# Kernel tuning notes

Measured on AMD Instinct MI355X. Metric: run time of the kernel, lower is better.

## Reference

```python
import jax, jax.numpy as jnp
import numpy as np

NH = 4
TEMP = 0.5

def _ln(x, w, b):
    mu = x.mean(-1, keepdims=True)
    var = ((x - mu) ** 2).mean(-1, keepdims=True)
    return (x - mu) / jnp.sqrt(var + 1e-5) * w + b

def _encoder(x, bias, key_pad, layers):
    # pre-LN torch TransformerEncoder, relu FFN, dropout=0
    Wqkv, bqkv, Wo, bo, ln1w, ln1b, ln2w, ln2b, W1, b1, W2, b2 = layers
    B, L, H = x.shape
    d = H // NH
    scale = 1.0 / np.sqrt(d)
    for i in range(Wqkv.shape[0]):
        y = _ln(x, ln1w[i], ln1b[i])
        qkv = y @ Wqkv[i].T + bqkv[i]
        q, k, v = jnp.split(qkv, 3, axis=-1)
        q = q.reshape(B, L, NH, d).transpose(0, 2, 1, 3)
        k = k.reshape(B, L, NH, d).transpose(0, 2, 1, 3)
        v = v.reshape(B, L, NH, d).transpose(0, 2, 1, 3)
        s = jnp.einsum('bhqd,bhkd->bhqk', q, k) * scale
        if bias is not None:
            s = s + bias
        s = s + key_pad[:, None, None, :]
        a = jax.nn.softmax(s, axis=-1)
        o = jnp.einsum('bhqk,bhkd->bhqd', a, v).transpose(0, 2, 1, 3).reshape(B, L, H)
        x = x + o @ Wo[i].T + bo[i]
        y = _ln(x, ln2w[i], ln2b[i])
        x = x + jax.nn.relu(y @ W1[i].T + b1[i]) @ W2[i].T + b2[i]
    return x

def _layer_params(key, nl, H, F, sc=0.05):
    ks = jax.random.split(key, 4)
    return (jax.random.normal(ks[0], (nl, 3 * H, H)) * sc, jnp.zeros((nl, 3 * H)),
            jax.random.normal(ks[1], (nl, H, H)) * sc, jnp.zeros((nl, H)),
            jnp.ones((nl, H)), jnp.zeros((nl, H)), jnp.ones((nl, H)), jnp.zeros((nl, H)),
            jax.random.normal(ks[2], (nl, F, H)) * sc, jnp.zeros((nl, F)),
            jax.random.normal(ks[3], (nl, H, F)) * sc, jnp.zeros((nl, H)))

def setup_inputs():
    key = jax.random.key(0)
    IN, H, ED, F = 64, 128, 16, 256
    G, NPG = 8, 512
    N = G * NPG
    m, k = 4, 16
    T = N
    S = T * m
    EPS = 24
    E_loc = S * EPS
    E = 65536
    ks = jax.random.split(key, 13)
    x = jax.random.normal(ks[0], (N, IN))
    log_probs = -jnp.abs(jax.random.normal(ks[1], (S,)))
    root = jnp.repeat(jnp.arange(T), m)
    base = (root // NPG) * NPG
    rest = base[:, None] + jax.random.randint(ks[2], (S, k - 1), 0, NPG)
    nodes_sampled = jnp.concatenate([root[:, None], rest], axis=1)
    valid = jnp.ones((S * k,), dtype=bool)
    edge_index_sampled = jax.random.randint(ks[3], (2, E_loc), 0, k)
    edge_ptr = jnp.arange(S + 1) * EPS
    ea_flat = jax.random.normal(ks[4], (E_loc, ED))
    src = jax.random.randint(ks[5], (E,), 0, N)
    dst = (src // NPG) * NPG + jax.random.randint(ks[6], (E,), 0, NPG)
    edge_index = jnp.stack([src, dst])
    edge_attr = jax.random.normal(ks[7], (E, ED))
    batch_vec = jnp.arange(N) // NPG
    ptr = jnp.arange(G + 1) * NPG
    d = dict(x=x, log_probs=log_probs, ea_flat=ea_flat, edge_attr=edge_attr,
             init_W=jax.random.normal(ks[8], (H, IN + 2)) * 0.05, init_b=jnp.zeros((H,)),
             loc_ep_W=jax.random.normal(ks[9], (NH, ED)) * 0.05, loc_ep_b=jnp.zeros((NH,)),
             glob_ep_W=jax.random.normal(ks[10], (NH, ED)) * 0.05, glob_ep_b=jnp.zeros((NH,)),
             loc_nw=jnp.ones((H,)), loc_nb=jnp.zeros((H,)),
             glob_nw=jnp.ones((H,)), glob_nb=jnp.zeros((H,)),
             nodes_sampled=nodes_sampled, edge_index_sampled=edge_index_sampled,
             edge_ptr=edge_ptr, edge_index=edge_index, batch_vec=batch_vec,
             ptr=ptr, valid=valid)
    names = ['Wqkv', 'bqkv', 'Wo', 'bo', 'ln1w', 'ln1b', 'ln2w', 'ln2b', 'W1', 'b1', 'W2', 'b2']
    for n, a in zip(names, _layer_params(ks[11], 4, H, F)):
        d['loc_' + n] = a
    for n, a in zip(names, _layer_params(ks[12], 4, H, F)):
        d['glob_' + n] = a
    return d

def reference(x, log_probs, ea_flat, edge_attr, init_W, init_b, loc_ep_W, loc_ep_b,
              glob_ep_W, glob_ep_b, loc_nw, loc_nb, glob_nw, glob_nb,
              loc_Wqkv, loc_bqkv, loc_Wo, loc_bo, loc_ln1w, loc_ln1b, loc_ln2w, loc_ln2b,
              loc_W1, loc_b1, loc_W2, loc_b2,
              glob_Wqkv, glob_bqkv, glob_Wo, glob_bo, glob_ln1w, glob_ln1b, glob_ln2w, glob_ln2b,
              glob_W1, glob_b1, glob_W2, glob_b2,
              nodes_sampled, edge_index_sampled, edge_ptr, edge_index, batch_vec, ptr, valid):
    S, k = nodes_sampled.shape
    N = x.shape[0]
    T = N
    m = S // T
    G = ptr.shape[0] - 1
    max_N = N // G  # equal-size graphs
    H = init_W.shape[0]
    # ---- phase 1: flatten subgraphs + init features ----
    x_flat = x[nodes_sampled.reshape(-1)]                         # [S*k, IN]
    root_global = jnp.repeat(jnp.arange(T), m)                    # [S]
    root_local = jnp.argmax(nodes_sampled == root_global[:, None], axis=1)
    root_mask = jnp.zeros((S * k,), x.dtype).at[jnp.arange(S) * k + root_local].set(1.0)
    lp = jnp.where(jnp.isfinite(log_probs), log_probs, 0.0)
    lp_flat = jnp.repeat(lp, k)[:, None] * valid[:, None].astype(x.dtype)
    h = jnp.concatenate([x_flat, lp_flat, root_mask[:, None]], axis=1) @ init_W.T + init_b
    # ---- local edge bias (scatter-add) ----
    E_loc = ea_flat.shape[0]
    sub = jnp.searchsorted(edge_ptr, jnp.arange(E_loc), side='right') - 1
    eap = ea_flat @ loc_ep_W.T + loc_ep_b                         # [E_loc, NH]
    lbias = jnp.zeros((S, k, k, NH), x.dtype).at[sub, edge_index_sampled[0], edge_index_sampled[1]].add(eap).transpose(0, 3, 1, 2)
    v2 = valid.reshape(S, k)
    key_pad_l = jnp.where(v2, 0.0, -1e9).astype(x.dtype)
    loc_layers = (loc_Wqkv, loc_bqkv, loc_Wo, loc_bo, loc_ln1w, loc_ln1b, loc_ln2w, loc_ln2b, loc_W1, loc_b1, loc_W2, loc_b2)
    out = _encoder(h.reshape(S, k, H), lbias, key_pad_l, loc_layers)
    out = _ln(out, loc_nw, loc_nb)
    vf = v2.astype(x.dtype)[..., None]
    sub_embs = (out * vf).sum(1) / jnp.maximum(vf.sum(1), 1.0)    # [S, H]
    # ---- weighted-mean aggregation over m samples per target node ----
    w = jax.nn.softmax(log_probs.reshape(T, m) / TEMP, axis=1)
    node_embs = jnp.einsum('tm,tmh->th', w, sub_embs.reshape(T, m, H))
    # ---- global phase: to_dense_batch + edge-bias transformer ----
    pos = jnp.arange(N) - ptr[batch_vec]
    dense = jnp.zeros((G, max_N, H), x.dtype).at[batch_vec, pos].set(node_embs)
    vmask = jnp.zeros((G, max_N), bool).at[batch_vec, pos].set(True)
    g = batch_vec[edge_index[0]]
    sl = edge_index[0] - ptr[g]
    dl = edge_index[1] - ptr[g]
    eag = edge_attr @ glob_ep_W.T + glob_ep_b
    gbias = jnp.zeros((G, max_N, max_N, NH), x.dtype).at[g, sl, dl].add(eag).transpose(0, 3, 1, 2)
    key_pad_g = jnp.where(vmask, 0.0, -1e9).astype(x.dtype)
    glob_layers = (glob_Wqkv, glob_bqkv, glob_Wo, glob_bo, glob_ln1w, glob_ln1b, glob_ln2w, glob_ln2b, glob_W1, glob_b1, glob_W2, glob_b2)
    gout = _encoder(dense, gbias, key_pad_g, glob_layers)
    gout = _ln(gout, glob_nw, glob_nb)
    return (gout * vmask[..., None].astype(x.dtype)).sum(1)      # [G, H]
```

## Files before the change

kernel.cpp:

```cpp
#include <hip/hip_runtime.h>
#include <math.h>

#define IN_F      64
#define H_DIM     128
#define NH_       4
#define DH_       32
#define FF_DIM    256
#define KSUB      16
#define S_SEQ     16384
#define E_LOC     393216
#define G_NUM     8
#define NPG_      512
#define N_NODES   4096
#define E_GLOB    65536
#define NLAYERS   4
#define SCALE_ATT 0.17677669529663687f

#define WQKV_SZ   (3*H_DIM*H_DIM)
#define WO_SZ     (H_DIM*H_DIM)
#define W1_SZ     (FF_DIM*H_DIM)
#define W2_SZ     (H_DIM*FF_DIM)

#define ATT(sg)   (4352 + (sg) * 2560)
#define PS_OFF    9472
#define STG_SZ    10112

typedef __bf16 bf16x8 __attribute__((ext_vector_type(8)));
typedef float  f32x4  __attribute__((ext_vector_type(4)));

__device__ __forceinline__ unsigned short f2bf(float f) {
    unsigned u = __float_as_uint(f);
    unsigned r = (u + 0x7fffu + ((u >> 16) & 1u)) >> 16;
    return (unsigned short)r;
}

__device__ __forceinline__ unsigned cvt_pk(float lo, float hi) {
    unsigned r;
    asm("v_cvt_pk_bf16_f32 %0, %1, %2" : "=v"(r) : "v"(lo), "v"(hi));
    return r;
}

__device__ __forceinline__ f32x4 mfma16(bf16x8 a, bf16x8 b, f32x4 c) {
    return __builtin_amdgcn_mfma_f32_16x16x32_bf16(a, b, c, 0, 0, 0);
}

#define PRIO_HI() __builtin_amdgcn_s_setprio(1)
#define PRIO_LO() __builtin_amdgcn_s_setprio(0)

__device__ __forceinline__ void ln_to_row(const float (&X)[8][4],
    const float* __restrict__ w, const float* __restrict__ b,
    unsigned short* rowb, int r, int q)
{
    float s1[4] = {0,0,0,0}, s2[4] = {0,0,0,0};
    #pragma unroll
    for (int t = 0; t < 8; ++t)
        #pragma unroll
        for (int i = 0; i < 4; ++i) { float v = X[t][i]; s1[i] += v; s2[i] += v*v; }
    #pragma unroll
    for (int i = 0; i < 4; ++i) {
        float a = s1[i], c = s2[i];
        a += __shfl_xor(a, 1, 16); a += __shfl_xor(a, 2, 16);
        a += __shfl_xor(a, 4, 16); a += __shfl_xor(a, 8, 16);
        c += __shfl_xor(c, 1, 16); c += __shfl_xor(c, 2, 16);
        c += __shfl_xor(c, 4, 16); c += __shfl_xor(c, 8, 16);
        float mu = a * (1.f / H_DIM);
        float var = c * (1.f / H_DIM) - mu * mu;
        s1[i] = mu; s2[i] = rsqrtf(fmaxf(var, 0.f) + 1e-5f);
    }
    for (int t = 0; t < 8; ++t) {
        float wv = w[t * 16 + r], bv = b[t * 16 + r];
        float v0 = (X[t][0] - s1[0]) * s2[0] * wv + bv;
        float v1 = (X[t][1] - s1[1]) * s2[1] * wv + bv;
        float v2 = (X[t][2] - s1[2]) * s2[2] * wv + bv;
        float v3 = (X[t][3] - s1[3]) * s2[3] * wv + bv;
        unsigned lo = cvt_pk(v0, v1), hi = cvt_pk(v2, v3);
        rowb[(q * 4 + 0) * 136 + t * 16 + r] = (unsigned short)lo;
        rowb[(q * 4 + 1) * 136 + t * 16 + r] = (unsigned short)(lo >> 16);
        rowb[(q * 4 + 2) * 136 + t * 16 + r] = (unsigned short)hi;
        rowb[(q * 4 + 3) * 136 + t * 16 + r] = (unsigned short)(hi >> 16);
    }
}

__device__ __forceinline__ void ln_mean_out(const float (&X)[8][4],
    const float* __restrict__ fnw, const float* __restrict__ fnb,
    float* __restrict__ dst, int r, int q)
{
    float s1[4] = {0,0,0,0}, s2[4] = {0,0,0,0};
    #pragma unroll
    for (int t = 0; t < 8; ++t)
        #pragma unroll
        for (int i = 0; i < 4; ++i) { float v = X[t][i]; s1[i] += v; s2[i] += v*v; }
    #pragma unroll
    for (int i = 0; i < 4; ++i) {
        float a = s1[i], c = s2[i];
        a += __shfl_xor(a, 1, 16); a += __shfl_xor(a, 2, 16);
        a += __shfl_xor(a, 4, 16); a += __shfl_xor(a, 8, 16);
        c += __shfl_xor(c, 1, 16); c += __shfl_xor(c, 2, 16);
        c += __shfl_xor(c, 4, 16); c += __shfl_xor(c, 8, 16);
        float mu = a * (1.f / H_DIM);
        float var = c * (1.f / H_DIM) - mu * mu;
        s1[i] = mu; s2[i] = rsqrtf(fmaxf(var, 0.f) + 1e-5f);
    }
    float colsum[8];
    #pragma unroll
    for (int t = 0; t < 8; ++t) {
        float wv = fnw[t * 16 + r], bv = fnb[t * 16 + r];
        float cs = 0.f;
        #pragma unroll
        for (int i = 0; i < 4; ++i) cs += (X[t][i] - s1[i]) * s2[i] * wv + bv;
        cs += __shfl_xor(cs, 16, 64);
        cs += __shfl_xor(cs, 32, 64);
        colsum[t] = cs;
    }
    float c0 = (q == 0) ? colsum[0] : (q == 1) ? colsum[1] : (q == 2) ? colsum[2] : colsum[3];
    float c1 = (q == 0) ? colsum[4] : (q == 1) ? colsum[5] : (q == 2) ? colsum[6] : colsum[7];
    dst[q * 16 + r]       = c0 * (1.f / KSUB);
    dst[(q + 4) * 16 + r] = c1 * (1.f / KSUB);
}

__global__ __launch_bounds__(256) void conv_all_k(
    const float* __restrict__ lWqkv, const float* __restrict__ lWo,
    const float* __restrict__ lW1, const float* __restrict__ lW2,
    const float* __restrict__ x,
    const float* __restrict__ gWqkv, const float* __restrict__ gWo,
    const float* __restrict__ gW1, const float* __restrict__ gW2,
    const float* __restrict__ init_W,
    unsigned short* __restrict__ wq_b, unsigned short* __restrict__ wo_b,
    unsigned short* __restrict__ w1_b, unsigned short* __restrict__ w2_b,
    unsigned short* __restrict__ x_b,
    unsigned short* __restrict__ gwq_b, unsigned short* __restrict__ gwo_b,
    unsigned short* __restrict__ gw1_b, unsigned short* __restrict__ gw2_b,
    unsigned short* __restrict__ wi_b)
{
    int b = blockIdx.x, t = threadIdx.x;
    const float* src; unsigned short* dst; int base;
    if (b < 768)       { src = lWqkv; dst = wq_b;  base = b; }
    else if (b < 1024) { src = lWo;   dst = wo_b;  base = b - 768; }
    else if (b < 1536) { src = lW1;   dst = w1_b;  base = b - 1024; }
    else if (b < 2048) { src = lW2;   dst = w2_b;  base = b - 1536; }
    else if (b < 3072) { src = x;     dst = x_b;   base = b - 2048; }
    else if (b < 3840) { src = gWqkv; dst = gwq_b; base = b - 3072; }
    else if (b < 4096) { src = gWo;   dst = gwo_b; base = b - 3840; }
    else if (b < 4608) { src = gW1;   dst = gw1_b; base = b - 4096; }
    else if (b < 5120) { src = gW2;   dst = gw2_b; base = b - 4608; }
    else {
        int i = (b - 5120) * 256 + t;
        int row = i >> 6, c = i & 63;
        wi_b[i] = f2bf(init_W[row * 66 + c]);
        return;
    }
    int i = base * 256 + t;
    dst[i] = f2bf(src[i]);
}

__global__ __launch_bounds__(64) void local_encoder_k(
    const unsigned short* __restrict__ xb16,
    const float* __restrict__ log_probs,
    const float* __restrict__ ea_flat,
    const float* __restrict__ init_W,
    const float* __restrict__ init_b,
    const unsigned short* __restrict__ wi_b,
    const float* __restrict__ ep_W, const float* __restrict__ ep_b,
    const int* __restrict__ nodes, const int* __restrict__ eis,
    const unsigned short* __restrict__ wqb, const unsigned short* __restrict__ wob,
    const unsigned short* __restrict__ w1b, const unsigned short* __restrict__ w2b,
    const float* __restrict__ bqkv, const float* __restrict__ bo,
    const float* __restrict__ ln1w, const float* __restrict__ ln1b,
    const float* __restrict__ ln2w, const float* __restrict__ ln2b,
    const float* __restrict__ b1, const float* __restrict__ b2,
    const float* __restrict__ fnw, const float* __restrict__ fnb,
    float* __restrict__ sub_embs)
{
    __shared__ unsigned short stg[STG_SZ];

    const int lane = threadIdx.x & 63;
    const int r = lane & 15, q = lane >> 4;
    const int s0 = blockIdx.x * 2;
    float* biasWrk = (float*)(stg + 4352);

    {
        float2 z2f; z2f.x = 0.f; z2f.y = 0.f;
        for (int i = lane; i < 1024; i += 64) ((float2*)biasWrk)[i] = z2f;
        uint4 z4; z4.x = 0; z4.y = 0; z4.z = 0; z4.w = 0;
        for (int i = lane; i < 80; i += 64) ((uint4*)(stg + PS_OFF))[i] = z4;
    }

    int ndA = nodes[s0 * KSUB + r];
    int ndB = nodes[(s0 + 1) * KSUB + r];
    int rootA = s0 >> 2, rootB = (s0 + 1) >> 2;
    unsigned long long balA = __ballot((q == 0) && (ndA == rootA));
    unsigned long long balB = __ballot((q == 0) && (ndB == rootB));
    int rjA = balA ? (__ffsll((long long)balA) - 1) : 0;
    int rjB = balB ? (__ffsll((long long)balB) - 1) : 0;
    float lpA = log_probs[s0];     if (!isfinite(lpA)) lpA = 0.f;
    float lpB = log_probs[s0 + 1]; if (!isfinite(lpB)) lpB = 0.f;

    if (lane < 48) {
        int ls = lane / 24, ee = lane % 24;
        int e = (s0 + ls) * 24 + ee;
        int i0 = eis[e], i1 = eis[E_LOC + e];
        const float* ea = ea_flat + (size_t)e * 16;
        float4 e0 = *(const float4*)(ea), e1 = *(const float4*)(ea + 4);
        float4 e2 = *(const float4*)(ea + 8), e3 = *(const float4*)(ea + 12);
        #pragma unroll
        for (int h = 0; h < NH_; ++h) {
            const float* wp = ep_W + h * 16;
            float v = ep_b[h]
                + e0.x * wp[0]  + e0.y * wp[1]  + e0.z * wp[2]  + e0.w * wp[3]
                + e1.x * wp[4]  + e1.y * wp[5]  + e1.z * wp[6]  + e1.w * wp[7]
                + e2.x * wp[8]  + e2.y * wp[9]  + e2.z * wp[10] + e2.w * wp[11]
                + e3.x * wp[12] + e3.y * wp[13] + e3.z * wp[14] + e3.w * wp[15];
            atomicAdd(&biasWrk[ls * 1024 + (h * 16 + i0) * 16 + i1], v);
        }
    }

    for (int i2 = lane; i2 < 256; i2 += 64) {
        int sg = i2 >> 7, row = (i2 >> 3) & 15, seg = i2 & 7;
        int nd = __shfl(sg ? ndB : ndA, row, 64);
        *(uint4*)(stg + sg * 2176 + row * 136 + seg * 8) =
            *(const uint4*)(xb16 + (size_t)nd * IN_F + seg * 8);
    }

    float bT[2][NH_][4];
    #pragma unroll
    for (int sg = 0; sg < 2; ++sg)
        #pragma unroll
        for (int h = 0; h < NH_; ++h)
            #pragma unroll
            for (int i = 0; i < 4; ++i)
                bT[sg][h][i] = biasWrk[sg * 1024 + (h * 16 + q * 4 + i) * 16 + r];

    {
        uint2 z2; z2.x = 0; z2.y = 0;
        for (int i = lane; i < 320; i += 64) ((uint2*)(stg + ATT(0) + 1280))[i] = z2;
        for (int i = lane; i < 320; i += 64) ((uint2*)(stg + ATT(1) + 1280))[i] = z2;
    }

    float X[2][8][4];
    {
        bf16x8 aA0 = *(const bf16x8*)(stg + r * 136 + q * 8);
        bf16x8 aA1 = *(const bf16x8*)(stg + r * 136 + 32 + q * 8);
        bf16x8 aB0 = *(const bf16x8*)(stg + 2176 + r * 136 + q * 8);
        bf16x8 aB1 = *(const bf16x8*)(stg + 2176 + r * 136 + 32 + q * 8);
        const unsigned short* wr0 = wi_b + (size_t)r * 64 + q * 8;
        bf16x8 c0 = *(const bf16x8*)(wr0);
        bf16x8 c1 = *(const bf16x8*)(wr0 + 32);
        for (int t = 0; t < 8; ++t) {
            bf16x8 n0, n1;
            if (t < 7) {
                const unsigned short* wn = wr0 + (t + 1) * 1024;
                n0 = *(const bf16x8*)(wn);
                n1 = *(const bf16x8*)(wn + 32);
            }
            f32x4 accA = {0.f,0.f,0.f,0.f}, accB = {0.f,0.f,0.f,0.f};
            PRIO_HI();
            accA = mfma16(aA0, c0, accA); accA = mfma16(aA1, c1, accA);
            accB = mfma16(aB0, c0, accB); accB = mfma16(aB1, c1, accB);
            PRIO_LO();
            int o = t * 16 + r;
            float w64 = init_W[o * 66 + 64], w65 = init_W[o * 66 + 65], bb = init_b[o];
            #pragma unroll
            for (int i = 0; i < 4; ++i) {
                float vA = accA[i] + lpA * w64 + bb;
                float vB = accB[i] + lpB * w64 + bb;
                if (q * 4 + i == rjA) vA += w65;
                if (q * 4 + i == rjB) vB += w65;
                X[0][t][i] = vA; X[1][t][i] = vB;
            }
            c0 = n0; c1 = n1;
        }
    }

    for (int l = 0; l < NLAYERS; ++l) {
        const unsigned short* wq_l = wqb + (size_t)l * WQKV_SZ;
        const unsigned short* wo_l = wob + (size_t)l * WO_SZ;
        const unsigned short* w1_l = w1b + (size_t)l * W1_SZ;
        const unsigned short* w2_l = w2b + (size_t)l * W2_SZ;

        ln_to_row(X[0], ln1w + l * H_DIM, ln1b + l * H_DIM, stg, r, q);
        ln_to_row(X[1], ln1w + l * H_DIM, ln1b + l * H_DIM, stg + 2176, r, q);
        bf16x8 af[2][4];
        #pragma unroll
        for (int sg = 0; sg < 2; ++sg)
            #pragma unroll
            for (int kt = 0; kt < 4; ++kt)
                af[sg][kt] = *(const bf16x8*)(stg + sg * 2176 + r * 136 + kt * 32 + q * 8);

        for (int h = 0; h < NH_; ++h) {
            #pragma unroll
            for (int t = 0; t < 2; ++t) {
                #pragma unroll
                for (int p = 0; p < 3; ++p) {
                    const unsigned short* wr =
                        wq_l + (size_t)(p * H_DIM + h * DH_ + t * 16 + r) * H_DIM + q * 8;
                    bf16x8 c0 = *(const bf16x8*)(wr);
                    bf16x8 c1 = *(const bf16x8*)(wr + 32);
                    bf16x8 c2 = *(const bf16x8*)(wr + 64);
                    bf16x8 c3 = *(const bf16x8*)(wr + 96);
                    f32x4 aA = {0.f,0.f,0.f,0.f}, aB = {0.f,0.f,0.f,0.f};
                    PRIO_HI();
                    aA = mfma16(af[0][0], c0, aA); aB = mfma16(af[1][0], c0, aB);
                    aA = mfma16(af[0][1], c1, aA); aB = mfma16(af[1][1], c1, aB);
                    aA = mfma16(af[0][2], c2, aA); aB = mfma16(af[1][2], c2, aB);
                    aA = mfma16(af[0][3], c3, aA); aB = mfma16(af[1][3], c3, aB);
                    PRIO_LO();
                    float bb = bqkv[l * 384 + p * H_DIM + h * DH_ + t * 16 + r];
                    if (p < 2) {
                        int off = p * 640;
                        unsigned la = cvt_pk(aA[0] + bb, aA[1] + bb);
                        unsigned ha = cvt_pk(aA[2] + bb, aA[3] + bb);
                        unsigned lb = cvt_pk(aB[0] + bb, aB[1] + bb);
                        unsigned hb = cvt_pk(aB[2] + bb, aB[3] + bb);
                        stg[ATT(0) + off + (q * 4 + 0) * 40 + t * 16 + r] = (unsigned short)la;
                        stg[ATT(0) + off + (q * 4 + 1) * 40 + t * 16 + r] = (unsigned short)(la >> 16);
                        stg[ATT(0) + off + (q * 4 + 2) * 40 + t * 16 + r] = (unsigned short)ha;
                        stg[ATT(0) + off + (q * 4 + 3) * 40 + t * 16 + r] = (unsigned short)(ha >> 16);
                        stg[ATT(1) + off + (q * 4 + 0) * 40 + t * 16 + r] = (unsigned short)lb;
                        stg[ATT(1) + off + (q * 4 + 1) * 40 + t * 16 + r] = (unsigned short)(lb >> 16);
                        stg[ATT(1) + off + (q * 4 + 2) * 40 + t * 16 + r] = (unsigned short)hb;
                        stg[ATT(1) + off + (q * 4 + 3) * 40 + t * 16 + r] = (unsigned short)(hb >> 16);
                    } else {
                        uint2 pkA, pkB;
                        pkA.x = cvt_pk(aA[0] + bb, aA[1] + bb);
                        pkA.y = cvt_pk(aA[2] + bb, aA[3] + bb);
                        pkB.x = cvt_pk(aB[0] + bb, aB[1] + bb);
                        pkB.y = cvt_pk(aB[2] + bb, aB[3] + bb);
                        *(uint2*)(stg + ATT(0) + 1280 + (t * 16 + r) * 40 + q * 4) = pkA;
                        *(uint2*)(stg + ATT(1) + 1280 + (t * 16 + r) * 40 + q * 4) = pkB;
                    }
                }
            }
            #pragma unroll
            for (int sg = 0; sg < 2; ++sg) {
                const int ab = ATT(sg);
                bf16x8 aq = *(const bf16x8*)(stg + ab + r * 40 + q * 8);
                bf16x8 bk = *(const bf16x8*)(stg + ab + 640 + r * 40 + q * 8);
                PRIO_HI();
                f32x4 sc = mfma16(aq, bk, (f32x4){0.f,0.f,0.f,0.f});
                PRIO_LO();
                float pvv[4];
                #pragma unroll
                for (int i = 0; i < 4; ++i) {
                    float e = __expf(sc[i] * SCALE_ATT + bT[sg][h][i]);
                    float sum = e;
                    sum += __shfl_xor(sum, 1, 16); sum += __shfl_xor(sum, 2, 16);
                    sum += __shfl_xor(sum, 4, 16); sum += __shfl_xor(sum, 8, 16);
                    pvv[i] = e * __builtin_amdgcn_rcpf(sum);
                }
                unsigned plo = cvt_pk(pvv[0], pvv[1]);
                unsigned phi = cvt_pk(pvv[2], pvv[3]);
                stg[PS_OFF + (q * 4 + 0) * 40 + r] = (unsigned short)plo;
                stg[PS_OFF + (q * 4 + 1) * 40 + r] = (unsigned short)(plo >> 16);
                stg[PS_OFF + (q * 4 + 2) * 40 + r] = (unsigned short)phi;
                stg[PS_OFF + (q * 4 + 3) * 40 + r] = (unsigned short)(phi >> 16);
                bf16x8 ap = *(const bf16x8*)(stg + PS_OFF + r * 40 + q * 8);
                #pragma unroll
                for (int t = 0; t < 2; ++t) {
                    bf16x8 bv = *(const bf16x8*)(stg + ab + 1280 + (t * 16 + r) * 40 + q * 8);
                    PRIO_HI();
                    f32x4 o = mfma16(ap, bv, (f32x4){0.f,0.f,0.f,0.f});
                    PRIO_LO();
                    unsigned olo = cvt_pk(o[0], o[1]);
                    unsigned ohi = cvt_pk(o[2], o[3]);
                    stg[sg * 2176 + (q * 4 + 0) * 136 + h * DH_ + t * 16 + r] = (unsigned short)olo;
                    stg[sg * 2176 + (q * 4 + 1) * 136 + h * DH_ + t * 16 + r] = (unsigned short)(olo >> 16);
                    stg[sg * 2176 + (q * 4 + 2) * 136 + h * DH_ + t * 16 + r] = (unsigned short)ohi;
                    stg[sg * 2176 + (q * 4 + 3) * 136 + h * DH_ + t * 16 + r] = (unsigned short)(ohi >> 16);
                }
            }
        }

        {
            bf16x8 ao[2][4];
            #pragma unroll
            for (int sg = 0; sg < 2; ++sg)
                #pragma unroll
                for (int kt = 0; kt < 4; ++kt)
                    ao[sg][kt] = *(const bf16x8*)(stg + sg * 2176 + r * 136 + kt * 32 + q * 8);
            const unsigned short* wr0 = wo_l + (size_t)r * H_DIM + q * 8;
            bf16x8 co[4], no[4];
            #pragma unroll
            for (int kt = 0; kt < 4; ++kt) co[kt] = *(const bf16x8*)(wr0 + kt * 32);
            for (int nt = 0; nt < 8; ++nt) {
                if (nt < 7) {
                    const unsigned short* wn = wr0 + (size_t)(nt + 1) * 2048;
                    #pragma unroll
                    for (int kt = 0; kt < 4; ++kt) no[kt] = *(const bf16x8*)(wn + kt * 32);
                }
                f32x4 aA = {0.f,0.f,0.f,0.f}, aB = {0.f,0.f,0.f,0.f};
                PRIO_HI();
                #pragma unroll
                for (int kt = 0; kt < 4; ++kt) {
                    aA = mfma16(ao[0][kt], co[kt], aA);
                    aB = mfma16(ao[1][kt], co[kt], aB);
                }
                PRIO_LO();
                float bov = bo[l * H_DIM + nt * 16 + r];
                #pragma unroll
                for (int i = 0; i < 4; ++i) {
                    X[0][nt][i] += aA[i] + bov;
                    X[1][nt][i] += aB[i] + bov;
                }
                #pragma unroll
                for (int kt = 0; kt < 4; ++kt) co[kt] = no[kt];
            }
        }

        ln_to_row(X[0], ln2w + l * H_DIM, ln2b + l * H_DIM, stg, r, q);
        ln_to_row(X[1], ln2w + l * H_DIM, ln2b + l * H_DIM, stg + 2176, r, q);

        {
            bf16x8 a2[2][4];
            #pragma unroll
            for (int sg = 0; sg < 2; ++sg)
                #pragma unroll
                for (int kt = 0; kt < 4; ++kt)
                    a2[sg][kt] = *(const bf16x8*)(stg + sg * 2176 + r * 136 + kt * 32 + q * 8);
            const unsigned short* wr0 = w1_l + (size_t)r * H_DIM + q * 8;
            bf16x8 c1b[4], n1b[4];
            #pragma unroll
            for (int kt = 0; kt < 4; ++kt) c1b[kt] = *(const bf16x8*)(wr0 + kt * 32);
            for (int nt = 0; nt < 16; ++nt) {
                if (nt < 15) {
                    const unsigned short* wn = wr0 + (size_t)(nt + 1) * 2048;
                    #pragma unroll
                    for (int kt = 0; kt < 4; ++kt) n1b[kt] = *(const bf16x8*)(wn + kt * 32);
                }
                float b1v = b1[l * FF_DIM + nt * 16 + r];
                #pragma unroll
                for (int sg = 0; sg < 2; ++sg) {
                    f32x4 acc = {0.f,0.f,0.f,0.f};
                    PRIO_HI();
                    #pragma unroll
                    for (int kt = 0; kt < 4; ++kt) acc = mfma16(a2[sg][kt], c1b[kt], acc);
                    PRIO_LO();
                    float f0 = fmaxf(acc[0] + b1v, 0.f), f1 = fmaxf(acc[1] + b1v, 0.f);
                    float f2 = fmaxf(acc[2] + b1v, 0.f), f3 = fmaxf(acc[3] + b1v, 0.f);
                    unsigned flo = cvt_pk(f0, f1), fhi = cvt_pk(f2, f3);
                    stg[sg * 4224 + (q * 4 + 0) * 264 + nt * 16 + r] = (unsigned short)flo;
                    stg[sg * 4224 + (q * 4 + 1) * 264 + nt * 16 + r] = (unsigned short)(flo >> 16);
                    stg[sg * 4224 + (q * 4 + 2) * 264 + nt * 16 + r] = (unsigned short)fhi;
                    stg[sg * 4224 + (q * 4 + 3) * 264 + nt * 16 + r] = (unsigned short)(fhi >> 16);
                }
                #pragma unroll
                for (int kt = 0; kt < 4; ++kt) c1b[kt] = n1b[kt];
            }
            for (int kp = 0; kp < 2; ++kp) {
                bf16x8 a1[2][4];
                #pragma unroll
                for (int sg = 0; sg < 2; ++sg)
                    #pragma unroll
                    for (int kt = 0; kt < 4; ++kt)
                        a1[sg][kt] = *(const bf16x8*)(stg + sg * 4224 + r * 264 + kp * 128 + kt * 32 + q * 8);
                const unsigned short* wr2 = w2_l + (size_t)r * FF_DIM + kp * 128 + q * 8;
                bf16x8 c2b[4], n2b[4];
                #pragma unroll
                for (int kt = 0; kt < 4; ++kt) c2b[kt] = *(const bf16x8*)(wr2 + kt * 32);
                for (int nt = 0; nt < 8; ++nt) {
                    if (nt < 7) {
                        const unsigned short* wn = wr2 + (size_t)(nt + 1) * 4096;
                        #pragma unroll
                        for (int kt = 0; kt < 4; ++kt) n2b[kt] = *(const bf16x8*)(wn + kt * 32);
                    }
                    f32x4 aA = {0.f,0.f,0.f,0.f}, aB = {0.f,0.f,0.f,0.f};
                    PRIO_HI();
                    #pragma unroll
                    for (int kt = 0; kt < 4; ++kt) {
                        aA = mfma16(a1[0][kt], c2b[kt], aA);
                        aB = mfma16(a1[1][kt], c2b[kt], aB);
                    }
                    PRIO_LO();
                    float b2v = (kp == 0) ? b2[l * H_DIM + nt * 16 + r] : 0.f;
                    #pragma unroll
                    for (int i = 0; i < 4; ++i) {
                        X[0][nt][i] += aA[i] + b2v;
                        X[1][nt][i] += aB[i] + b2v;
                    }
                    #pragma unroll
                    for (int kt = 0; kt < 4; ++kt) c2b[kt] = n2b[kt];
                }
            }
        }
    }

    ln_mean_out(X[0], fnw, fnb, sub_embs + (size_t)s0 * H_DIM, r, q);
    ln_mean_out(X[1], fnw, fnb, sub_embs + (size_t)(s0 + 1) * H_DIM, r, q);
}

__global__ __launch_bounds__(256) void agg_ln_k(const float* __restrict__ sub,
    const float* __restrict__ lp, const int* __restrict__ bvec,
    const int* __restrict__ ptrg, const float* __restrict__ w,
    const float* __restrict__ b, float* __restrict__ xg,
    unsigned short* __restrict__ yout)
{
    int t = blockIdx.x * 16 + (threadIdx.x >> 4);
    int ln = threadIdx.x & 15;
    float l0 = lp[t * 4 + 0] * 2.f, l1 = lp[t * 4 + 1] * 2.f;
    float l2 = lp[t * 4 + 2] * 2.f, l3 = lp[t * 4 + 3] * 2.f;
    float mx = fmaxf(fmaxf(l0, l1), fmaxf(l2, l3));
    float e0 = __expf(l0 - mx), e1 = __expf(l1 - mx);
    float e2 = __expf(l2 - mx), e3 = __expf(l3 - mx);
    float inv = 1.f / (e0 + e1 + e2 + e3);
    e0 *= inv; e1 *= inv; e2 *= inv; e3 *= inv;
    int g = bvec[t];
    int row = g * NPG_ + (t - ptrg[g]);
    const float* sp = sub + (size_t)t * 4 * H_DIM;
    float v[8], s1 = 0.f, s2 = 0.f;
    #pragma unroll
    for (int k = 0; k < 8; ++k) {
        int i = ln + k * 16;
        float val = e0 * sp[i] + e1 * sp[H_DIM + i] + e2 * sp[2 * H_DIM + i]
                  + e3 * sp[3 * H_DIM + i];
        xg[(size_t)row * H_DIM + i] = val;
        v[k] = val; s1 += val; s2 += val * val;
    }
    for (int m2 = 8; m2 >= 1; m2 >>= 1) {
        s1 += __shfl_xor(s1, m2, 16);
        s2 += __shfl_xor(s2, m2, 16);
    }
    float mu = s1 * (1.f / H_DIM), var = s2 * (1.f / H_DIM) - mu * mu;
    float rs = rsqrtf(fmaxf(var, 0.f) + 1e-5f);
    #pragma unroll
    for (int k = 0; k < 8; ++k) {
        int i = ln + k * 16;
        yout[(size_t)row * H_DIM + i] = f2bf((v[k] - mu) * rs * w[i] + b[i]);
    }
}

__global__ __launch_bounds__(256) void zero_k(float4* __restrict__ p)
{
    p[(size_t)blockIdx.x * 256 + threadIdx.x] = make_float4(0.f, 0.f, 0.f, 0.f);
}

__global__ __launch_bounds__(256) void gbias_scatter_k(
    const float* __restrict__ edge_attr, const int* __restrict__ eidx,
    const int* __restrict__ bvec, const int* __restrict__ ptrg,
    const float* __restrict__ epW, const float* __restrict__ epb,
    float* __restrict__ gbias)
{
    int e = blockIdx.x * 256 + threadIdx.x;
    int src = eidx[e], dst = eidx[E_GLOB + e];
    int g = bvec[src];
    int sl = src - ptrg[g], dl = dst - ptrg[g];
    const float* ea = edge_attr + (size_t)e * 16;
    #pragma unroll
    for (int h = 0; h < NH_; ++h) {
        float v = epb[h];
        #pragma unroll
        for (int t = 0; t < 16; ++t) v += ea[t] * epW[h * 16 + t];
        atomicAdd(&gbias[(((size_t)g * NH_ + h) * NPG_ + sl) * NPG_ + dl], v);
    }
}

__global__ __launch_bounds__(64) void attn_fused_k(
    const unsigned short* __restrict__ qkv,
    const unsigned short* __restrict__ vt,
    const float* __restrict__ gbias,
    unsigned short* __restrict__ attg)
{
    __shared__ unsigned short pbuf[16 * 522];
    const int lane = threadIdx.x & 63;
    const int r = lane & 15, q = lane >> 4;
    const int qt = blockIdx.x, z = blockIdx.y;
    const int g = z >> 2, h = z & 3;
    const int qrow0 = qt * 16;

    bf16x8 fq = *(const bf16x8*)(qkv + (size_t)(g * NPG_ + qrow0 + r) * 384
                                 + h * DH_ + q * 8);
    const float* gb = gbias + (size_t)z * NPG_ * NPG_ + (size_t)qrow0 * NPG_;
    const unsigned short* kbase = qkv + (size_t)g * NPG_ * 384 + H_DIM + h * DH_ + q * 8;

    float mx[4] = {-1e30f, -1e30f, -1e30f, -1e30f};
    for (int kt = 0; kt < 32; ++kt) {
        bf16x8 bk = *(const bf16x8*)(kbase + (size_t)(kt * 16 + r) * 384);
        f32x4 sc = mfma16(fq, bk, (f32x4){0.f,0.f,0.f,0.f});
        #pragma unroll
        for (int i = 0; i < 4; ++i)
            mx[i] = fmaxf(mx[i],
                sc[i] * SCALE_ATT + gb[(size_t)(q * 4 + i) * NPG_ + kt * 16 + r]);
    }
    #pragma unroll
    for (int i = 0; i < 4; ++i) {
        mx[i] = fmaxf(mx[i], __shfl_xor(mx[i], 1, 16));
        mx[i] = fmaxf(mx[i], __shfl_xor(mx[i], 2, 16));
        mx[i] = fmaxf(mx[i], __shfl_xor(mx[i], 4, 16));
        mx[i] = fmaxf(mx[i], __shfl_xor(mx[i], 8, 16));
    }

    float sm[4] = {0.f, 0.f, 0.f, 0.f};
    for (int kt = 0; kt < 32; ++kt) {
        bf16x8 bk = *(const bf16x8*)(kbase + (size_t)(kt * 16 + r) * 384);
        f32x4 sc = mfma16(fq, bk, (f32x4){0.f,0.f,0.f,0.f});
        float e0 = __expf(sc[0] * SCALE_ATT + gb[(size_t)(q * 4 + 0) * NPG_ + kt * 16 + r] - mx[0]);
        float e1 = __expf(sc[1] * SCALE_ATT + gb[(size_t)(q * 4 + 1) * NPG_ + kt * 16 + r] - mx[1]);
        float e2 = __expf(sc[2] * SCALE_ATT + gb[(size_t)(q * 4 + 2) * NPG_ + kt * 16 + r] - mx[2]);
        float e3 = __expf(sc[3] * SCALE_ATT + gb[(size_t)(q * 4 + 3) * NPG_ + kt * 16 + r] - mx[3]);
        sm[0] += e0; sm[1] += e1; sm[2] += e2; sm[3] += e3;
        unsigned lo = cvt_pk(e0, e1), hi = cvt_pk(e2, e3);
        pbuf[(q * 4 + 0) * 522 + kt * 16 + r] = (unsigned short)lo;
        pbuf[(q * 4 + 1) * 522 + kt * 16 + r] = (unsigned short)(lo >> 16);
        pbuf[(q * 4 + 2) * 522 + kt * 16 + r] = (unsigned short)hi;
        pbuf[(q * 4 + 3) * 522 + kt * 16 + r] = (unsigned short)(hi >> 16);
    }
    float inv[4];
    #pragma unroll
    for (int i = 0; i < 4; ++i) {
        float s = sm[i];
        s += __shfl_xor(s, 1, 16); s += __shfl_xor(s, 2, 16);
        s += __shfl_xor(s, 4, 16); s += __shfl_xor(s, 8, 16);
        inv[i] = 1.f / s;
    }

    f32x4 oa = {0.f,0.f,0.f,0.f}, ob = {0.f,0.f,0.f,0.f};
    const unsigned short* v0p = vt + (size_t)(z * 32 + r) * NPG_;
    const unsigned short* v1p = vt + (size_t)(z * 32 + 16 + r) * NPG_;
    for (int kc = 0; kc < 16; ++kc) {
        bf16x8 ap  = *(const bf16x8*)(pbuf + r * 522 + kc * 32 + q * 8);
        bf16x8 bv0 = *(const bf16x8*)(v0p + kc * 32 + q * 8);
        bf16x8 bv1 = *(const bf16x8*)(v1p + kc * 32 + q * 8);
        oa = mfma16(ap, bv0, oa);
        ob = mfma16(ap, bv1, ob);
    }
    #pragma unroll
    for (int i = 0; i < 4; ++i) {
        size_t row = (size_t)(g * NPG_ + qrow0 + q * 4 + i) * H_DIM + h * DH_;
        attg[row + r]      = f2bf(oa[i] * inv[i]);
        attg[row + 16 + r] = f2bf(ob[i] * inv[i]);
    }
}

__global__ __launch_bounds__(256) void gemm_mfma_k(
    const unsigned short* __restrict__ A, const unsigned short* __restrict__ B,
    void* __restrict__ Cv, const float* __restrict__ bias, const float* __restrict__ D,
    unsigned short* __restrict__ vtout,
    int M, int N, int K, int lda, int ldb, int ldc, int ldd,
    long sAg, long sAh, long sBg, long sBh, long sCg, long sCh, long sDg, long sDh,
    float alpha, int op)
{
    const int z = blockIdx.z, zg = z >> 2, zh = z & 3;
    A += zg * sAg + zh * sAh;
    B += zg * sBg + zh * sBh;
    const int lane = threadIdx.x & 63, wave = threadIdx.x >> 6;
    const int r = lane & 15, q = lane >> 4;
    const int m0 = blockIdx.y * 64 + wave * 16;
    const int n0 = blockIdx.x * 64;
    const int ntiles = min(4, (N - n0) >> 4);
    const int KT = K >> 5;
    const unsigned short* ap = A + (size_t)(m0 + r) * lda + q * 8;
    for (int nt = 0; nt < ntiles; ++nt) {
        const int col = n0 + nt * 16 + r;
        const unsigned short* bp = B + (size_t)col * ldb + q * 8;
        f32x4 acc = {0.f, 0.f, 0.f, 0.f};
        for (int kc = 0; kc < KT; ++kc) {
            bf16x8 av = *(const bf16x8*)(ap + kc * 32);
            bf16x8 bv = *(const bf16x8*)(bp + kc * 32);
            acc = mfma16(av, bv, acc);
        }
        float bv2 = bias ? bias[col] : 0.f;
        #pragma unroll
        for (int i = 0; i < 4; ++i) {
            const int row = m0 + q * 4 + i;
            if (op == 0) {
                ((unsigned short*)Cv)[zg * sCg + zh * sCh + (size_t)row * ldc + col] =
                    f2bf(acc[i] + bv2);
            } else if (op == 1) {
                ((float*)Cv)[zg * sCg + zh * sCh + (size_t)row * ldc + col] =
                    alpha * acc[i] + (D ? D[zg * sDg + zh * sDh + (size_t)row * ldd + col] : 0.f);
            } else if (op == 3) {
                ((unsigned short*)Cv)[(size_t)row * ldc + col] = f2bf(fmaxf(acc[i] + bv2, 0.f));
            } else {
                unsigned short hv = f2bf(acc[i] + bv2);
                ((unsigned short*)Cv)[(size_t)row * ldc + col] = hv;
                if (col >= 256) {
                    int h = (col - 256) >> 5, d = (col - 256) & 31;
                    int g = row >> 9, tok = row & 511;
                    vtout[(((size_t)(g * 4 + h)) * 32 + d) * 512 + tok] = hv;
                }
            }
        }
    }
}

template <int KT>
__global__ __launch_bounds__(64) void gemm_ln_k(
    const unsigned short* __restrict__ A, const unsigned short* __restrict__ B,
    const float* __restrict__ bias, float* __restrict__ xg,
    const float* __restrict__ lnw, const float* __restrict__ lnb,
    void* __restrict__ yout, int mode)
{
    const int lane = threadIdx.x & 63;
    const int r = lane & 15, q = lane >> 4;
    const int m0 = blockIdx.x * 16;
    const int K = KT * 32;
    const unsigned short* ap = A + (size_t)(m0 + r) * K + q * 8;
    bf16x8 afr[KT];
    #pragma unroll
    for (int kc = 0; kc < KT; ++kc) afr[kc] = *(const bf16x8*)(ap + kc * 32);
    float v[8][4];
    #pragma unroll
    for (int nt = 0; nt < 8; ++nt) {
        const int col = nt * 16 + r;
        const unsigned short* bp = B + (size_t)col * K + q * 8;
        f32x4 acc = {0.f, 0.f, 0.f, 0.f};
        #pragma unroll
        for (int kc = 0; kc < KT; ++kc)
            acc = mfma16(afr[kc], *(const bf16x8*)(bp + kc * 32), acc);
        float bb = bias[col];
        #pragma unroll
        for (int i = 0; i < 4; ++i) {
            const int row = m0 + q * 4 + i;
            float nv = xg[(size_t)row * H_DIM + col] + acc[i] + bb;
            xg[(size_t)row * H_DIM + col] = nv;
            v[nt][i] = nv;
        }
    }
    float s1[4] = {0,0,0,0}, s2[4] = {0,0,0,0};
    #pragma unroll
    for (int nt = 0; nt < 8; ++nt)
        #pragma unroll
        for (int i = 0; i < 4; ++i) { float x = v[nt][i]; s1[i] += x; s2[i] += x * x; }
    #pragma unroll
    for (int i = 0; i < 4; ++i) {
        float a = s1[i], c = s2[i];
        a += __shfl_xor(a, 1, 16); a += __shfl_xor(a, 2, 16);
        a += __shfl_xor(a, 4, 16); a += __shfl_xor(a, 8, 16);
        c += __shfl_xor(c, 1, 16); c += __shfl_xor(c, 2, 16);
        c += __shfl_xor(c, 4, 16); c += __shfl_xor(c, 8, 16);
        float mu = a * (1.f / H_DIM);
        float var = c * (1.f / H_DIM) - mu * mu;
        s1[i] = mu; s2[i] = rsqrtf(fmaxf(var, 0.f) + 1e-5f);
    }
    #pragma unroll
    for (int nt = 0; nt < 8; ++nt) {
        const int col = nt * 16 + r;
        float wv = lnw[col], bv = lnb[col];
        #pragma unroll
        for (int i = 0; i < 4; ++i) {
            const int row = m0 + q * 4 + i;
            float ln = (v[nt][i] - s1[i]) * s2[i] * wv + bv;
            if (mode == 0) ((unsigned short*)yout)[(size_t)row * H_DIM + col] = f2bf(ln);
            else           ((float*)yout)[(size_t)row * H_DIM + col] = ln;
        }
    }
}

__global__ __launch_bounds__(1024) void reduce_out_k(const float* __restrict__ yg,
                                                     float* __restrict__ out)
{
    __shared__ float part[8][128];
    int g = blockIdx.x;
    int i = threadIdx.x & 127, c = threadIdx.x >> 7;
    float s = 0.f;
    const float* base = yg + ((size_t)(g * NPG_ + c * 64)) * H_DIM + i;
    for (int t = 0; t < 64; ++t) s += base[(size_t)t * H_DIM];
    part[c][i] = s;
    __syncthreads();
    if (threadIdx.x < 128) {
        float acc = 0.f;
        #pragma unroll
        for (int c2 = 0; c2 < 8; ++c2) acc += part[c2][threadIdx.x];
        out[g * H_DIM + threadIdx.x] = acc;
    }
}

static inline void launch_gmm(hipStream_t st, const unsigned short* A, const unsigned short* B,
    void* C, const float* bias, const float* D, unsigned short* vt,
    int M, int N, int K, int lda, int ldb, int ldc, int ldd,
    long sAg, long sAh, long sBg, long sBh, long sCg, long sCh, long sDg, long sDh,
    float alpha, int op, int Z)
{
    dim3 grid((N + 63) / 64, M / 64, Z);
    hipLaunchKernelGGL(gemm_mfma_k, grid, dim3(256), 0, st, A, B, C, bias, D, vt,
        M, N, K, lda, ldb, ldc, ldd, sAg, sAh, sBg, sBh, sCg, sCh, sDg, sDh, alpha, op);
}

extern "C" void kernel_launch(void* const* d_in, const int* in_sizes, int n_in,
                              void* d_out, int out_size, void* d_ws, size_t ws_size,
                              hipStream_t stream)
{
    const float* x         = (const float*)d_in[0];
    const float* lp        = (const float*)d_in[1];
    const float* ea_flat   = (const float*)d_in[2];
    const float* edge_attr = (const float*)d_in[3];
    const float* init_W    = (const float*)d_in[4];
    const float* init_b    = (const float*)d_in[5];
    const float* lepW      = (const float*)d_in[6];
    const float* lepb      = (const float*)d_in[7];
    const float* gepW      = (const float*)d_in[8];
    const float* gepb      = (const float*)d_in[9];
    const float* lnw       = (const float*)d_in[10];
    const float* lnb       = (const float*)d_in[11];
    const float* gnw       = (const float*)d_in[12];
    const float* gnb       = (const float*)d_in[13];
    const int*   nodes     = (const int*)d_in[14];
    const int*   eis       = (const int*)d_in[15];
    const int*   eptr      = (const int*)d_in[16];  (void)eptr;
    const int*   eidx      = (const int*)d_in[17];
    const int*   bvec      = (const int*)d_in[18];
    const int*   ptrg      = (const int*)d_in[19];
    const float* lWqkv = (const float*)d_in[21];
    const float* lbqkv = (const float*)d_in[22];
    const float* lWo   = (const float*)d_in[23];
    const float* lbo   = (const float*)d_in[24];
    const float* lln1w = (const float*)d_in[25];
    const float* lln1b = (const float*)d_in[26];
    const float* lln2w = (const float*)d_in[27];
    const float* lln2b = (const float*)d_in[28];
    const float* lW1   = (const float*)d_in[29];
    const float* lb1   = (const float*)d_in[30];
    const float* lW2   = (const float*)d_in[31];
    const float* lb2   = (const float*)d_in[32];
    const float* gWqkv = (const float*)d_in[33];
    const float* gbqkv = (const float*)d_in[34];
    const float* gWo   = (const float*)d_in[35];
    const float* gbo   = (const float*)d_in[36];
    const float* gln1w = (const float*)d_in[37];
    const float* gln1b = (const float*)d_in[38];
    const float* gln2w = (const float*)d_in[39];
    const float* gln2b = (const float*)d_in[40];
    const float* gW1   = (const float*)d_in[41];
    const float* gb1   = (const float*)d_in[42];
    const float* gW2   = (const float*)d_in[43];
    const float* gb2   = (const float*)d_in[44];

    float* out = (float*)d_out;
    float* ws  = (float*)d_ws;
    float* gbias   = ws;
    float* scores  = ws + 8388608;
    float* subembs = scores;
    float* xg      = ws + 16777216;
    unsigned short* qkvg_b = (unsigned short*)(ws + 17301504);
    unsigned short* yg_b   = (unsigned short*)(ws + 18087936);
    unsigned short* attg_b = (unsigned short*)(ws + 18350080);
    unsigned short* ffg_b  = (unsigned short*)(ws + 18612224);
    unsigned short* vt_b   = (unsigned short*)(ws + 19136512);
    unsigned short* gw     = (unsigned short*)(ws + 19398656);

    unsigned short* wb   = (unsigned short*)gbias;
    unsigned short* wq_b = wb;
    unsigned short* wo_b = wb + 196608;
    unsigned short* w1_b = wb + 262144;
    unsigned short* w2_b = wb + 393216;
    unsigned short* x_b  = wb + 524288;
    unsigned short* wi_b = wb + 786432;
    unsigned short* gwq_b = gw;
    unsigned short* gwo_b = gw + 196608;
    unsigned short* gw1_b = gw + 262144;
    unsigned short* gw2_b = gw + 393216;

    hipLaunchKernelGGL(conv_all_k, dim3(5152), dim3(256), 0, stream,
        lWqkv, lWo, lW1, lW2, x, gWqkv, gWo, gW1, gW2, init_W,
        wq_b, wo_b, w1_b, w2_b, x_b, gwq_b, gwo_b, gw1_b, gw2_b, wi_b);

    hipLaunchKernelGGL(local_encoder_k, dim3(S_SEQ / 2), dim3(64), 0, stream,
        x_b, lp, ea_flat, init_W, init_b, wi_b, lepW, lepb, nodes, eis,
        wq_b, wo_b, w1_b, w2_b,
        lbqkv, lbo, lln1w, lln1b, lln2w, lln2b, lb1, lb2,
        lnw, lnb, subembs);

    hipLaunchKernelGGL(agg_ln_k, dim3(N_NODES / 16), dim3(256), 0, stream,
        subembs, lp, bvec, ptrg, gln1w, gln1b, xg, yg_b);

    hipLaunchKernelGGL(zero_k, dim3(8192), dim3(256), 0, stream, (float4*)gbias);
    hipLaunchKernelGGL(gbias_scatter_k, dim3(E_GLOB / 256), dim3(256), 0, stream,
        edge_attr, eidx, bvec, ptrg, gepW, gepb, gbias);

    for (int l = 0; l < NLAYERS; ++l) {
        launch_gmm(stream, yg_b, gwq_b + (size_t)l * WQKV_SZ, qkvg_b,
                   gbqkv + l * 384, nullptr, vt_b, 4096, 384, 128, 128, 128, 384, 0,
                   0, 0, 0, 0, 0, 0, 0, 0, 1.f, 4, 1);
        hipLaunchKernelGGL(attn_fused_k, dim3(NPG_ / 16, 32), dim3(64), 0, stream,
            qkvg_b, vt_b, gbias, attg_b);
        hipLaunchKernelGGL(gemm_ln_k<4>, dim3(256), dim3(64), 0, stream,
            attg_b, gwo_b + (size_t)l * WO_SZ, gbo + l * H_DIM, xg,
            gln2w + l * H_DIM, gln2b + l * H_DIM, (void*)yg_b, 0);
        launch_gmm(stream, yg_b, gw1_b + (size_t)l * W1_SZ, ffg_b,
                   gb1 + l * FF_DIM, nullptr, nullptr, 4096, 256, 128, 128, 128, 256, 0,
                   0, 0, 0, 0, 0, 0, 0, 0, 1.f, 3, 1);
        const float* nw = (l < 3) ? (gln1w + (l + 1) * H_DIM) : gnw;
        const float* nb = (l < 3) ? (gln1b + (l + 1) * H_DIM) : gnb;
        void* yo = (l < 3) ? (void*)yg_b : (void*)scores;
        hipLaunchKernelGGL(gemm_ln_k<8>, dim3(256), dim3(64), 0, stream,
            ffg_b, gw2_b + (size_t)l * W2_SZ, gb2 + l * H_DIM, xg,
            nw, nb, yo, (l < 3) ? 0 : 1);
    }

    hipLaunchKernelGGL(reduce_out_k, dim3(G_NUM), dim3(1024), 0, stream, scores, out);
}
```

Baseline: 1.387 ms.

## Fuse global layer tail (Wo+LN2+FFN+LN) into one per-row-tile kernel

Replaces the three per-layer launches (Wo GEMM with LN, FFN1 GEMM, FFN2 GEMM with LN) in the global encoder with a single kernel. Each 64-thread block keeps a 16-row residual tile in registers and stages the LN2 output and the ReLU FFN hidden in shared memory, so the FFN intermediate never goes to global memory. Weight fragments are software-prefetched one tile ahead, with MFMA priority hints. In exchange there are fewer launches and less DRAM traffic, but only 256 single-wave blocks, so the GPU may be underfilled and the per-block serial work is longer.

```diff
diff --git a/kernel.cpp b/kernel.cpp
--- a/kernel.cpp
+++ b/kernel.cpp
@@ -663,11 +663,6 @@
             if (op == 0) {
                 ((unsigned short*)Cv)[zg * sCg + zh * sCh + (size_t)row * ldc + col] =
                     f2bf(acc[i] + bv2);
-            } else if (op == 1) {
-                ((float*)Cv)[zg * sCg + zh * sCh + (size_t)row * ldc + col] =
-                    alpha * acc[i] + (D ? D[zg * sDg + zh * sDh + (size_t)row * ldd + col] : 0.f);
-            } else if (op == 3) {
-                ((unsigned short*)Cv)[(size_t)row * ldc + col] = f2bf(fmaxf(acc[i] + bv2, 0.f));
             } else {
                 unsigned short hv = f2bf(acc[i] + bv2);
                 ((unsigned short*)Cv)[(size_t)row * ldc + col] = hv;
@@ -681,44 +676,131 @@
     }
 }
 
-template <int KT>
-__global__ __launch_bounds__(64) void gemm_ln_k(
-    const unsigned short* __restrict__ A, const unsigned short* __restrict__ B,
-    const float* __restrict__ bias, float* __restrict__ xg,
-    const float* __restrict__ lnw, const float* __restrict__ lnb,
+__global__ __launch_bounds__(64) void layer_tail_k(
+    const unsigned short* __restrict__ attg,
+    const unsigned short* __restrict__ wo,
+    const unsigned short* __restrict__ w1,
+    const unsigned short* __restrict__ w2,
+    const float* __restrict__ bo, const float* __restrict__ b1,
+    const float* __restrict__ b2,
+    float* __restrict__ xg,
+    const float* __restrict__ ln2w, const float* __restrict__ ln2b,
+    const float* __restrict__ nw, const float* __restrict__ nb,
     void* __restrict__ yout, int mode)
 {
+    __shared__ unsigned short stg2[16 * 264];
     const int lane = threadIdx.x & 63;
     const int r = lane & 15, q = lane >> 4;
     const int m0 = blockIdx.x * 16;
-    const int K = KT * 32;
-    const unsigned short* ap = A + (size_t)(m0 + r) * K + q * 8;
-    bf16x8 afr[KT];
-    #pragma unroll
-    for (int kc = 0; kc < KT; ++kc) afr[kc] = *(const bf16x8*)(ap + kc * 32);
-    float v[8][4];
-    #pragma unroll
-    for (int nt = 0; nt < 8; ++nt) {
-        const int col = nt * 16 + r;
-        const unsigned short* bp = B + (size_t)col * K + q * 8;
-        f32x4 acc = {0.f, 0.f, 0.f, 0.f};
-        #pragma unroll
-        for (int kc = 0; kc < KT; ++kc)
-            acc = mfma16(afr[kc], *(const bf16x8*)(bp + kc * 32), acc);
-        float bb = bias[col];
-        #pragma unroll
-        for (int i = 0; i < 4; ++i) {
-            const int row = m0 + q * 4 + i;
-            float nv = xg[(size_t)row * H_DIM + col] + acc[i] + bb;
-            xg[(size_t)row * H_DIM + col] = nv;
-            v[nt][i] = nv;
-        }
-    }
+
+    float X[8][4];
+    #pragma unroll
+    for (int nt = 0; nt < 8; ++nt)
+        #pragma unroll
+        for (int i = 0; i < 4; ++i)
+            X[nt][i] = xg[(size_t)(m0 + q * 4 + i) * H_DIM + nt * 16 + r];
+
+    {
+        bf16x8 ao[4];
+        #pragma unroll
+        for (int kt = 0; kt < 4; ++kt)
+            ao[kt] = *(const bf16x8*)(attg + (size_t)(m0 + r) * H_DIM + kt * 32 + q * 8);
+        const unsigned short* wr0 = wo + (size_t)r * H_DIM + q * 8;
+        bf16x8 co[4], no[4];
+        #pragma unroll
+        for (int kt = 0; kt < 4; ++kt) co[kt] = *(const bf16x8*)(wr0 + kt * 32);
+        for (int nt = 0; nt < 8; ++nt) {
+            if (nt < 7) {
+                const unsigned short* wn = wr0 + (size_t)(nt + 1) * 2048;
+                #pragma unroll
+                for (int kt = 0; kt < 4; ++kt) no[kt] = *(const bf16x8*)(wn + kt * 32);
+            }
+            f32x4 acc = {0.f,0.f,0.f,0.f};
+            PRIO_HI();
+            #pragma unroll
+            for (int kt = 0; kt < 4; ++kt) acc = mfma16(ao[kt], co[kt], acc);
+            PRIO_LO();
+            float bov = bo[nt * 16 + r];
+            #pragma unroll
+            for (int i = 0; i < 4; ++i) X[nt][i] += acc[i] + bov;
+            #pragma unroll
+            for (int kt = 0; kt < 4; ++kt) co[kt] = no[kt];
+        }
+    }
+
+    ln_to_row(X, ln2w, ln2b, stg2, r, q);
+
+    {
+        bf16x8 a2[4];
+        #pragma unroll
+        for (int kt = 0; kt < 4; ++kt)
+            a2[kt] = *(const bf16x8*)(stg2 + r * 136 + kt * 32 + q * 8);
+        const unsigned short* wr0 = w1 + (size_t)r * H_DIM + q * 8;
+        bf16x8 c1b[4], n1b[4];
+        #pragma unroll
+        for (int kt = 0; kt < 4; ++kt) c1b[kt] = *(const bf16x8*)(wr0 + kt * 32);
+        for (int nt = 0; nt < 16; ++nt) {
+            if (nt < 15) {
+                const unsigned short* wn = wr0 + (size_t)(nt + 1) * 2048;
+                #pragma unroll
+                for (int kt = 0; kt < 4; ++kt) n1b[kt] = *(const bf16x8*)(wn + kt * 32);
+            }
+            float b1v = b1[nt * 16 + r];
+            f32x4 acc = {0.f,0.f,0.f,0.f};
+            PRIO_HI();
+            #pragma unroll
+            for (int kt = 0; kt < 4; ++kt) acc = mfma16(a2[kt], c1b[kt], acc);
+            PRIO_LO();
+            float f0 = fmaxf(acc[0] + b1v, 0.f), f1 = fmaxf(acc[1] + b1v, 0.f);
+            float f2 = fmaxf(acc[2] + b1v, 0.f), f3 = fmaxf(acc[3] + b1v, 0.f);
+            unsigned flo = cvt_pk(f0, f1), fhi = cvt_pk(f2, f3);
+            stg2[(q * 4 + 0) * 264 + nt * 16 + r] = (unsigned short)flo;
+            stg2[(q * 4 + 1) * 264 + nt * 16 + r] = (unsigned short)(flo >> 16);
+            stg2[(q * 4 + 2) * 264 + nt * 16 + r] = (unsigned short)fhi;
+            stg2[(q * 4 + 3) * 264 + nt * 16 + r] = (unsigned short)(fhi >> 16);
+            #pragma unroll
+            for (int kt = 0; kt < 4; ++kt) c1b[kt] = n1b[kt];
+        }
+        for (int kp = 0; kp < 2; ++kp) {
+            bf16x8 a1[4];
+            #pragma unroll
+            for (int kt = 0; kt < 4; ++kt)
+                a1[kt] = *(const bf16x8*)(stg2 + r * 264 + kp * 128 + kt * 32 + q * 8);
+            const unsigned short* wr2 = w2 + (size_t)r * FF_DIM + kp * 128 + q * 8;
+            bf16x8 c2b[4], n2b[4];
+            #pragma unroll
+            for (int kt = 0; kt < 4; ++kt) c2b[kt] = *(const bf16x8*)(wr2 + kt * 32);
+            for (int nt = 0; nt < 8; ++nt) {
+                if (nt < 7) {
+                    const unsigned short* wn = wr2 + (size_t)(nt + 1) * 4096;
+                    #pragma unroll
+                    for (int kt = 0; kt < 4; ++kt) n2b[kt] = *(const bf16x8*)(wn + kt * 32);
+                }
+                f32x4 acc = {0.f,0.f,0.f,0.f};
+                PRIO_HI();
+                #pragma unroll
+                for (int kt = 0; kt < 4; ++kt) acc = mfma16(a1[kt], c2b[kt], acc);
+                PRIO_LO();
+                float b2v = (kp == 0) ? b2[nt * 16 + r] : 0.f;
+                #pragma unroll
+                for (int i = 0; i < 4; ++i) X[nt][i] += acc[i] + b2v;
+                #pragma unroll
+                for (int kt = 0; kt < 4; ++kt) c2b[kt] = n2b[kt];
+            }
+        }
+    }
+
+    #pragma unroll
+    for (int nt = 0; nt < 8; ++nt)
+        #pragma unroll
+        for (int i = 0; i < 4; ++i)
+            xg[(size_t)(m0 + q * 4 + i) * H_DIM + nt * 16 + r] = X[nt][i];
+
     float s1[4] = {0,0,0,0}, s2[4] = {0,0,0,0};
     #pragma unroll
     for (int nt = 0; nt < 8; ++nt)
         #pragma unroll
-        for (int i = 0; i < 4; ++i) { float x = v[nt][i]; s1[i] += x; s2[i] += x * x; }
+        for (int i = 0; i < 4; ++i) { float x = X[nt][i]; s1[i] += x; s2[i] += x * x; }
     #pragma unroll
     for (int i = 0; i < 4; ++i) {
         float a = s1[i], c = s2[i];
@@ -733,11 +815,11 @@
     #pragma unroll
     for (int nt = 0; nt < 8; ++nt) {
         const int col = nt * 16 + r;
-        float wv = lnw[col], bv = lnb[col];
+        float wv = nw[col], bv = nb[col];
         #pragma unroll
         for (int i = 0; i < 4; ++i) {
             const int row = m0 + q * 4 + i;
-            float ln = (v[nt][i] - s1[i]) * s2[i] * wv + bv;
+            float ln = (X[nt][i] - s1[i]) * s2[i] * wv + bv;
             if (mode == 0) ((unsigned short*)yout)[(size_t)row * H_DIM + col] = f2bf(ln);
             else           ((float*)yout)[(size_t)row * H_DIM + col] = ln;
         }
@@ -761,17 +843,6 @@
         for (int c2 = 0; c2 < 8; ++c2) acc += part[c2][threadIdx.x];
         out[g * H_DIM + threadIdx.x] = acc;
     }
-}
-
-static inline void launch_gmm(hipStream_t st, const unsigned short* A, const unsigned short* B,
-    void* C, const float* bias, const float* D, unsigned short* vt,
-    int M, int N, int K, int lda, int ldb, int ldc, int ldd,
-    long sAg, long sAh, long sBg, long sBh, long sCg, long sCh, long sDg, long sDh,
-    float alpha, int op, int Z)
-{
-    dim3 grid((N + 63) / 64, M / 64, Z);
-    hipLaunchKernelGGL(gemm_mfma_k, grid, dim3(256), 0, st, A, B, C, bias, D, vt,
-        M, N, K, lda, ldb, ldc, ldd, sAg, sAh, sBg, sBh, sCg, sCh, sDg, sDh, alpha, op);
 }
 
 extern "C" void kernel_launch(void* const* d_in, const int* in_sizes, int n_in,
@@ -835,6 +906,7 @@
     unsigned short* ffg_b  = (unsigned short*)(ws + 18612224);
     unsigned short* vt_b   = (unsigned short*)(ws + 19136512);
     unsigned short* gw     = (unsigned short*)(ws + 19398656);
+    (void)ffg_b;
 
     unsigned short* wb   = (unsigned short*)gbias;
     unsigned short* wq_b = wb;
@@ -866,22 +938,23 @@
         edge_attr, eidx, bvec, ptrg, gepW, gepb, gbias);
 
     for (int l = 0; l < NLAYERS; ++l) {
-        launch_gmm(stream, yg_b, gwq_b + (size_t)l * WQKV_SZ, qkvg_b,
-                   gbqkv + l * 384, nullptr, vt_b, 4096, 384, 128, 128, 128, 384, 0,
-                   0, 0, 0, 0, 0, 0, 0, 0, 1.f, 4, 1);
+        {
+            dim3 grid((384 + 63) / 64, 4096 / 64, 1);
+            hipLaunchKernelGGL(gemm_mfma_k, grid, dim3(256), 0, stream,
+                yg_b, gwq_b + (size_t)l * WQKV_SZ, qkvg_b,
+                gbqkv + l * 384, nullptr, vt_b, 4096, 384, 128, 128, 128, 384, 0,
+                0, 0, 0, 0, 0, 0, 0, 0, 1.f, 4);
+        }
         hipLaunchKernelGGL(attn_fused_k, dim3(NPG_ / 16, 32), dim3(64), 0, stream,
             qkvg_b, vt_b, gbias, attg_b);
-        hipLaunchKernelGGL(gemm_ln_k<4>, dim3(256), dim3(64), 0, stream,
-            attg_b, gwo_b + (size_t)l * WO_SZ, gbo + l * H_DIM, xg,
-            gln2w + l * H_DIM, gln2b + l * H_DIM, (void*)yg_b, 0);
-        launch_gmm(stream, yg_b, gw1_b + (size_t)l * W1_SZ, ffg_b,
-                   gb1 + l * FF_DIM, nullptr, nullptr, 4096, 256, 128, 128, 128, 256, 0,
-                   0, 0, 0, 0, 0, 0, 0, 0, 1.f, 3, 1);
         const float* nw = (l < 3) ? (gln1w + (l + 1) * H_DIM) : gnw;
         const float* nb = (l < 3) ? (gln1b + (l + 1) * H_DIM) : gnb;
         void* yo = (l < 3) ? (void*)yg_b : (void*)scores;
-        hipLaunchKernelGGL(gemm_ln_k<8>, dim3(256), dim3(64), 0, stream,
-            ffg_b, gw2_b + (size_t)l * W2_SZ, gb2 + l * H_DIM, xg,
+        hipLaunchKernelGGL(layer_tail_k, dim3(N_NODES / 16), dim3(64), 0, stream,
+            attg_b, gwo_b + (size_t)l * WO_SZ, gw1_b + (size_t)l * W1_SZ,
+            gw2_b + (size_t)l * W2_SZ,
+            gbo + l * H_DIM, gb1 + l * FF_DIM, gb2 + l * H_DIM,
+            xg, gln2w + l * H_DIM, gln2b + l * H_DIM,
             nw, nb, yo, (l < 3) ? 0 : 1);
     }
 
```

After: 1.358 ms. 1.02x faster.
